# Optimization experiments

Hardware: AMD Instinct MI355X
Metric: run time of the kernel (lower is better)

The kernel has to match this reference:

```python
import jax, jax.numpy as jnp
from jax import lax
import numpy as np

C_IN = 64
C_OUT = 64
CQ = C_OUT // 8   # query/key channels
K = 5             # axial kernel length
RATIO = 0.7       # hybrid-norm mixing ratio
EPS = 1e-5
DN = ('NCHW', 'OIHW', 'NCHW')


def setup_inputs() -> dict:
    key = jax.random.key(0)
    ks = jax.random.split(key, 16)
    rn = lambda k, s, sc=0.05: jax.random.normal(k, s, dtype=jnp.float32) * sc
    return dict(
        x=jax.random.normal(ks[0], (4, C_IN, 256, 256), dtype=jnp.float32),
        hconv_w=rn(ks[1], (C_IN, 1, 1, K)), hconv_b=rn(ks[2], (C_IN,)),
        vconv_w=rn(ks[3], (C_IN, 1, K, 1)), vconv_b=rn(ks[4], (C_IN,)),
        pw_w=rn(ks[5], (C_OUT, C_IN)), pw_b=rn(ks[6], (C_OUT,)),
        bn_w=1.0 + rn(ks[7], (C_OUT,)), bn_b=rn(ks[8], (C_OUT,)),
        q_w=rn(ks[9], (CQ, C_OUT)), q_b=rn(ks[10], (CQ,)),
        k_w=rn(ks[11], (CQ, C_OUT)), k_b=rn(ks[12], (CQ,)),
        v_w=rn(ks[13], (C_OUT, C_OUT)), v_b=rn(ks[14], (C_OUT,)),
        gamma=rn(ks[15], (1,), 0.1),
    )


def reference(x, hconv_w, hconv_b, vconv_w, vconv_b, pw_w, pw_b,
              bn_w, bn_b, q_w, q_b, k_w, k_b, v_w, v_b, gamma):
    # ---- AxialDepthwiseConv: depthwise (1,K) + (K,1) + x, relu, pointwise ----
    h = lax.conv_general_dilated(x, hconv_w, (1, 1), [(0, 0), (K // 2, K // 2)],
                                 dimension_numbers=DN, feature_group_count=C_IN)
    h = h + hconv_b[:, None, None]
    v = lax.conv_general_dilated(x, vconv_w, (1, 1), [(K // 2, K // 2), (0, 0)],
                                 dimension_numbers=DN, feature_group_count=C_IN)
    v = v + vconv_b[:, None, None]
    a = jax.nn.relu(h + v + x)
    y = jnp.einsum('bchw,oc->bohw', a, pw_w) + pw_b[:, None, None]

    # ---- HybridNormalization: 0.7*InstanceNorm(no affine) + 0.3*BatchNorm(train) ----
    im = y.mean((2, 3), keepdims=True)
    iv = y.var((2, 3), keepdims=True)
    inn = (y - im) * lax.rsqrt(iv + EPS)
    bm = y.mean((0, 2, 3), keepdims=True)
    bv = y.var((0, 2, 3), keepdims=True)
    bnn = (y - bm) * lax.rsqrt(bv + EPS) * bn_w[:, None, None] + bn_b[:, None, None]
    y = RATIO * inn + (1.0 - RATIO) * bnn

    # ---- CrissCrossAttention ----
    q = jnp.einsum('bchw,oc->bohw', y, q_w) + q_b[:, None, None]   # (B,CQ,H,W)
    k = jnp.einsum('bchw,oc->bohw', y, k_w) + k_b[:, None, None]   # (B,CQ,H,W)
    val = jnp.einsum('bchw,oc->bohw', y, v_w) + v_b[:, None, None] # (B,C,H,W)

    # height (per column w): attn[b,w,j,i] = softmax_i( q[b,:,j,w] . k[b,:,i,w] )
    Ah = jax.nn.softmax(jnp.einsum('bcjw,bciw->bwji', q, k), axis=-1)
    # h_out[b,c,i,w] = sum_j val[b,c,j,w] * Ah[b,w,j,i]  (matches bmm(value, attn))
    h_out = jnp.einsum('bcjw,bwji->bciw', val, Ah)

    # width (per row h): attn[b,h,y,x] = softmax_x( q[b,:,h,y] . k[b,:,h,x] )
    Av = jax.nn.softmax(jnp.einsum('bchy,bchx->bhyx', q, k), axis=-1)
    v_out = jnp.einsum('bchy,bhyx->bchx', val, Av)

    out = gamma[0] * (h_out + v_out) + y

    # ---- MaxPool2d(2,2) ----
    down = lax.reduce_window(out, -jnp.inf, lax.max, (1, 1, 2, 2), (1, 1, 2, 2), 'VALID')
    return out, down
```

## Files before the change

kernel.cpp:

```cpp
#include <hip/hip_runtime.h>
#include <hip/hip_bf16.h>

#define Bn 4
#define Cc 64
#define CQn 8
#define Hh 256
#define Ww 256
#define PLANE 65536

typedef unsigned short ushortT;
typedef __attribute__((ext_vector_type(8))) unsigned short us8;
typedef __attribute__((ext_vector_type(4))) unsigned short us4;
typedef __attribute__((ext_vector_type(8))) __bf16 bf16x8;
typedef __attribute__((ext_vector_type(4))) float f32x4;

__device__ inline ushortT f2bf(float f) {
    __hip_bfloat16 h = __float2bfloat16(f);
    return *(ushortT*)&h;
}
__device__ inline float bf2f(ushortT u) {
    return __uint_as_float((unsigned)u << 16);
}
union BF8U { us8 u; bf16x8 b; uint4 w; };
__device__ inline us8 zero_us8() {
    BF8U z; z.w.x = 0; z.w.y = 0; z.w.z = 0; z.w.w = 0; return z.u;
}

__global__ __launch_bounds__(256) void dw_kernel(
    const float* __restrict__ x,
    const float* __restrict__ hw, const float* __restrict__ hb,
    const float* __restrict__ vw, const float* __restrict__ vb,
    ushortT* __restrict__ aout)
{
    int blk = blockIdx.x;
    int bc = blk >> 4;
    int ht = blk & 15;
    int h0 = ht * 16;
    int c = bc & 63;
    int tid = threadIdx.x;
    __shared__ float rows[20][260];
    const float* xp = x + (size_t)bc * PLANE;
    #pragma unroll
    for (int i = 0; i < 20; ++i) {
        int hr = h0 - 2 + i;
        rows[i][tid + 2] = (hr >= 0 && hr < Hh) ? xp[hr * Ww + tid] : 0.f;
    }
    if (tid < 20) {
        rows[tid][0] = 0.f; rows[tid][1] = 0.f;
        rows[tid][258] = 0.f; rows[tid][259] = 0.f;
    }
    __syncthreads();

    float hw0 = hw[c * 5 + 0], hw1 = hw[c * 5 + 1], hw2 = hw[c * 5 + 2],
          hw3 = hw[c * 5 + 3], hw4 = hw[c * 5 + 4];
    float vw0 = vw[c * 5 + 0], vw1 = vw[c * 5 + 1], vw2 = vw[c * 5 + 2],
          vw3 = vw[c * 5 + 3], vw4 = vw[c * 5 + 4];
    float bias = hb[c] + vb[c];

    ushortT* op = aout + (size_t)bc * PLANE + h0 * Ww + tid;
    #pragma unroll
    for (int r = 0; r < 16; ++r) {
        float hs = hw0 * rows[r + 2][tid]     + hw1 * rows[r + 2][tid + 1]
                 + hw2 * rows[r + 2][tid + 2] + hw3 * rows[r + 2][tid + 3]
                 + hw4 * rows[r + 2][tid + 4];
        float vs = vw0 * rows[r][tid + 2]     + vw1 * rows[r + 1][tid + 2]
                 + vw2 * rows[r + 2][tid + 2] + vw3 * rows[r + 3][tid + 2]
                 + vw4 * rows[r + 4][tid + 2];
        float res = hs + vs + bias + rows[r + 2][tid + 2];
        op[r * Ww] = f2bf(fmaxf(res, 0.f));
    }
}

__global__ __launch_bounds__(256) void pw_mfma_kernel(
    const ushortT* __restrict__ a_bf, const float* __restrict__ pwwf,
    const float* __restrict__ pwb,
    float* __restrict__ y_raw, float* __restrict__ sums, float* __restrict__ sumsq)
{
    int blk = blockIdx.x;
    int b = blk >> 8;
    int t0 = (blk & 255) << 8;
    int tid = threadIdx.x, lane = tid & 63, wv = tid >> 6;
    int half = lane >> 4;
    int col = lane & 15;

    __shared__ ushortT ytile[256 * 74];

    {
        size_t base = (size_t)b * Cc * PLANE + t0 + tid;
        uint* wrow = (uint*)&ytile[tid * 74];
        #pragma unroll
        for (int c = 0; c < Cc; c += 2) {
            ushortT v0 = a_bf[base + (size_t)c * PLANE];
            ushortT v1 = a_bf[base + (size_t)(c + 1) * PLANE];
            wrow[c >> 1] = (uint)v0 | ((uint)v1 << 16);
        }
    }
    __syncthreads();

    int m0 = wv * 16;
    BF8U a0, a1;
    {
        const float* wr = pwwf + (m0 + col) * 64 + half * 8;
        #pragma unroll
        for (int e = 0; e < 8; ++e) {
            a0.u[e] = f2bf(wr[e]);
            a1.u[e] = f2bf(wr[32 + e]);
        }
    }

    float bias[4], s[4], s2[4];
    #pragma unroll
    for (int r = 0; r < 4; ++r) {
        bias[r] = pwb[m0 + half * 4 + r];
        s[r] = 0.f; s2[r] = 0.f;
    }

    const uint* lw = (const uint*)ytile;
    #pragma unroll 4
    for (int t = 0; t < 16; ++t) {
        int rbase = (t * 16 + col) * 37 + half * 4;
        BF8U b0, b1;
        b0.w.x = lw[rbase];      b0.w.y = lw[rbase + 1];
        b0.w.z = lw[rbase + 2];  b0.w.w = lw[rbase + 3];
        b1.w.x = lw[rbase + 16]; b1.w.y = lw[rbase + 17];
        b1.w.z = lw[rbase + 18]; b1.w.w = lw[rbase + 19];
        f32x4 acc = (f32x4){0.f, 0.f, 0.f, 0.f};
        acc = __builtin_amdgcn_mfma_f32_16x16x32_bf16(a0.b, b0.b, acc, 0, 0, 0);
        acc = __builtin_amdgcn_mfma_f32_16x16x32_bf16(a1.b, b1.b, acc, 0, 0, 0);
        int pix = t * 16 + col;
        #pragma unroll
        for (int r = 0; r < 4; ++r) {
            int c = m0 + half * 4 + r;
            float v = acc[r] + bias[r];
            y_raw[(size_t)(b * Cc + c) * PLANE + t0 + pix] = v;
            s[r] += v; s2[r] += v * v;
        }
    }
    #pragma unroll
    for (int r = 0; r < 4; ++r) {
        #pragma unroll
        for (int d = 8; d > 0; d >>= 1) {
            s[r]  += __shfl_down(s[r], d, 16);
            s2[r] += __shfl_down(s2[r], d, 16);
        }
    }
    if (col == 0) {
        #pragma unroll
        for (int r = 0; r < 4; ++r) {
            int c = m0 + half * 4 + r;
            atomicAdd(&sums[b * Cc + c], s[r]);
            atomicAdd(&sumsq[b * Cc + c], s2[r]);
        }
    }
}

__global__ __launch_bounds__(256) void qkv_mfma_kernel(
    const float* __restrict__ y_raw,
    const float* __restrict__ sums, const float* __restrict__ sumsq,
    const float* __restrict__ bnw, const float* __restrict__ bnb,
    const float* __restrict__ qwf, const float* __restrict__ qbias,
    const float* __restrict__ kwf, const float* __restrict__ kbias,
    const float* __restrict__ vwf, const float* __restrict__ vbias,
    ushortT* __restrict__ q, ushortT* __restrict__ k,
    ushortT* __restrict__ val)
{
    int blk = blockIdx.x;
    int b = blk >> 8;
    int t0 = (blk & 255) << 8;
    int tid = threadIdx.x, lane = tid & 63, wv = tid >> 6;
    int half = lane >> 4;
    int col = lane & 15;

    __shared__ ushortT ytile[256 * 74];
    __shared__ float alpha_s[64], beta_s[64];

    if (tid < 64) {
        int c = tid;
        float im[4], e2[4];
        float bm = 0.f, be2 = 0.f;
        #pragma unroll
        for (int bb = 0; bb < 4; ++bb) {
            im[bb] = sums[bb * Cc + c] * (1.f / 65536.f);
            e2[bb] = sumsq[bb * Cc + c] * (1.f / 65536.f);
            bm += im[bb]; be2 += e2[bb];
        }
        bm *= 0.25f; be2 *= 0.25f;
        float rsb = rsqrtf(be2 - bm * bm + 1e-5f);
        float wgt = bnw[c];
        float rsi = rsqrtf(e2[b] - im[b] * im[b] + 1e-5f);
        alpha_s[c] = 0.7f * rsi + 0.3f * rsb * wgt;
        beta_s[c]  = -0.7f * im[b] * rsi - 0.3f * bm * rsb * wgt + 0.3f * bnb[c];
    }
    __syncthreads();

    {
        size_t base = (size_t)b * Cc * PLANE + t0 + tid;
        uint* wrow = (uint*)&ytile[tid * 74];
        #pragma unroll
        for (int c = 0; c < Cc; c += 2) {
            float v0 = y_raw[base + (size_t)c * PLANE];
            float v1 = y_raw[base + (size_t)(c + 1) * PLANE];
            float n0 = alpha_s[c] * v0 + beta_s[c];
            float n1 = alpha_s[c + 1] * v1 + beta_s[c + 1];
            wrow[c >> 1] = (uint)f2bf(n0) | ((uint)f2bf(n1) << 16);
        }
    }
    __syncthreads();

    const uint* lw = (const uint*)ytile;

    {
        const float* wr = (col < 8) ? (qwf + col * 64) : (kwf + (col - 8) * 64);
        BF8U a0, a1;
        #pragma unroll
        for (int e = 0; e < 8; ++e) {
            a0.u[e] = f2bf(wr[half * 8 + e]);
            a1.u[e] = f2bf(wr[32 + half * 8 + e]);
        }
        #pragma unroll
        for (int i = 0; i < 4; ++i) {
            int t = wv * 4 + i;
            int rbase = (t * 16 + col) * 37 + half * 4;
            BF8U b0, b1;
            b0.w.x = lw[rbase];      b0.w.y = lw[rbase + 1];
            b0.w.z = lw[rbase + 2];  b0.w.w = lw[rbase + 3];
            b1.w.x = lw[rbase + 16]; b1.w.y = lw[rbase + 17];
            b1.w.z = lw[rbase + 18]; b1.w.w = lw[rbase + 19];
            f32x4 acc = (f32x4){0.f, 0.f, 0.f, 0.f};
            acc = __builtin_amdgcn_mfma_f32_16x16x32_bf16(a0.b, b0.b, acc, 0, 0, 0);
            acc = __builtin_amdgcn_mfma_f32_16x16x32_bf16(a1.b, b1.b, acc, 0, 0, 0);
            int pix = t * 16 + col;
            #pragma unroll
            for (int r = 0; r < 4; ++r) {
                int row = half * 4 + r;
                if (row < 8)
                    q[(size_t)(b * CQn + row) * PLANE + t0 + pix] = f2bf(acc[r] + qbias[row]);
                else
                    k[(size_t)(b * CQn + row - 8) * PLANE + t0 + pix] = f2bf(acc[r] + kbias[row - 8]);
            }
        }
    }

    {
        int m0 = wv * 16;
        BF8U a0, a1;
        {
            const float* wr = vwf + (m0 + col) * 64 + half * 8;
            #pragma unroll
            for (int e = 0; e < 8; ++e) {
                a0.u[e] = f2bf(wr[e]);
                a1.u[e] = f2bf(wr[32 + e]);
            }
        }
        float bias[4];
        #pragma unroll
        for (int r = 0; r < 4; ++r) bias[r] = vbias[m0 + half * 4 + r];
        #pragma unroll 4
        for (int t = 0; t < 16; ++t) {
            int rbase = (t * 16 + col) * 37 + half * 4;
            BF8U b0, b1;
            b0.w.x = lw[rbase];      b0.w.y = lw[rbase + 1];
            b0.w.z = lw[rbase + 2];  b0.w.w = lw[rbase + 3];
            b1.w.x = lw[rbase + 16]; b1.w.y = lw[rbase + 17];
            b1.w.z = lw[rbase + 18]; b1.w.w = lw[rbase + 19];
            f32x4 acc = (f32x4){0.f, 0.f, 0.f, 0.f};
            acc = __builtin_amdgcn_mfma_f32_16x16x32_bf16(a0.b, b0.b, acc, 0, 0, 0);
            acc = __builtin_amdgcn_mfma_f32_16x16x32_bf16(a1.b, b1.b, acc, 0, 0, 0);
            int pix = t * 16 + col;
            #pragma unroll
            for (int r = 0; r < 4; ++r) {
                int c = m0 + half * 4 + r;
                val[(size_t)(b * Cc + c) * PLANE + t0 + pix] = f2bf(acc[r] + bias[r]);
            }
        }
    }
}

__global__ __launch_bounds__(256) void transpose_all_kernel(
    const ushortT* __restrict__ qb, ushortT* __restrict__ qT,
    const ushortT* __restrict__ kb, ushortT* __restrict__ kT,
    const ushortT* __restrict__ vb, ushortT* __restrict__ vT)
{
    int blk = blockIdx.x;
    int plane = blk >> 6;
    int tile = blk & 63;
    const ushortT* src; ushortT* dst;
    if (plane < 32)      { src = qb + (size_t)plane * PLANE;        dst = qT + (size_t)plane * PLANE; }
    else if (plane < 64) { src = kb + (size_t)(plane - 32) * PLANE; dst = kT + (size_t)(plane - 32) * PLANE; }
    else                 { src = vb + (size_t)(plane - 64) * PLANE; dst = vT + (size_t)(plane - 64) * PLANE; }
    int th = (tile >> 3) * 32;
    int tw = (tile & 7) * 32;
    __shared__ ushortT t[32][34];
    int lw = threadIdx.x & 31;
    int lh = threadIdx.x >> 5;
    #pragma unroll
    for (int i = 0; i < 4; ++i)
        t[lh + 8 * i][lw] = src[(th + lh + 8 * i) * Ww + tw + lw];
    __syncthreads();
    #pragma unroll
    for (int i = 0; i < 4; ++i)
        dst[(tw + lh + 8 * i) * Hh + th + lw] = t[lw][lh + 8 * i];
}

__global__ __launch_bounds__(256) void attn_kernel(
    const ushortT* __restrict__ q0, const ushortT* __restrict__ k0,
    const ushortT* __restrict__ v0, ushortT* __restrict__ o0,
    const ushortT* __restrict__ q1, const ushortT* __restrict__ k1,
    const ushortT* __restrict__ v1, ushortT* __restrict__ o1)
{
    int blk = blockIdx.x;
    int sel = blk >> 10;
    const ushortT* __restrict__ q   = sel ? q1 : q0;
    const ushortT* __restrict__ k   = sel ? k1 : k0;
    const ushortT* __restrict__ val = sel ? v1 : v0;
    ushortT* __restrict__ outp      = sel ? o1 : o0;
    int bblk = blk & 1023;
    int b = bblk >> 8;
    int r = bblk & 255;
    int tid = threadIdx.x;
    int lane = tid & 63;
    int wv = tid >> 6;
    int col = lane & 15;
    int quad = lane >> 4;

    __shared__ ushortT q_s[256 * 8];
    __shared__ ushortT k_s[256 * 8];
    __shared__ ushortT A_lds[4 * 256 * 8];
    __shared__ float mhat[256];
    __shared__ float shiftv[256];
    __shared__ float kred[32];

    size_t vbase = (size_t)b * Cc * PLANE + (size_t)r * Ww
                 + (size_t)(wv * 16 + col) * PLANE + quad * 8;
    BF8U afb[2];
    afb[0].u = *(const us8*)(val + vbase);

    size_t qkbase = (size_t)b * CQn * PLANE + (size_t)r * Ww + tid;
    float qf[8], ka[8];
    {
        BF8U qp, kp;
        #pragma unroll
        for (int c = 0; c < 8; ++c) {
            ushortT qv = q[qkbase + (size_t)c * PLANE];
            ushortT kv = k[qkbase + (size_t)c * PLANE];
            qp.u[c] = qv; kp.u[c] = kv;
            qf[c] = bf2f(qv);
            ka[c] = fabsf(bf2f(kv));
        }
        *(us8*)&q_s[tid * 8] = qp.u;
        *(us8*)&k_s[tid * 8] = kp.u;
    }
    #pragma unroll
    for (int d = 1; d < 64; d <<= 1)
        #pragma unroll
        for (int c = 0; c < 8; ++c)
            ka[c] = fmaxf(ka[c], __shfl_xor(ka[c], d));
    if (lane == 0)
        #pragma unroll
        for (int c = 0; c < 8; ++c) kred[wv * 8 + c] = ka[c];
    __syncthreads();

    {
        float mh = 0.f;
        #pragma unroll
        for (int c = 0; c < 8; ++c) {
            float km = fmaxf(fmaxf(kred[c], kred[8 + c]),
                             fmaxf(kred[16 + c], kred[24 + c]));
            mh += fabsf(qf[c]) * km;
        }
        mhat[tid] = mh;
    }
    __syncthreads();

    #pragma unroll
    for (int t = 0; t < 4; ++t) {
        int jt = wv * 4 + t;
        BF8U qa; qa.u = zero_us8();
        if (quad == 0) qa.u = *(const us8*)&q_s[(jt * 16 + col) * 8];
        float mh4[4];
        #pragma unroll
        for (int rr = 0; rr < 4; ++rr) mh4[rr] = mhat[jt * 16 + quad * 4 + rr];
        f32x4 ls = (f32x4){0.f, 0.f, 0.f, 0.f};
        for (int it = 0; it < 16; ++it) {
            BF8U kb;
            kb.u = *(const us8*)&k_s[(it * 16 + col) * 8];
            f32x4 sacc = (f32x4){0.f, 0.f, 0.f, 0.f};
            sacc = __builtin_amdgcn_mfma_f32_16x16x32_bf16(qa.b, kb.b, sacc, 0, 0, 0);
            #pragma unroll
            for (int rr = 0; rr < 4; ++rr)
                ls[rr] += __expf(sacc[rr] - mh4[rr]);
        }
        #pragma unroll
        for (int d = 1; d < 16; d <<= 1)
            #pragma unroll
            for (int rr = 0; rr < 4; ++rr)
                ls[rr] += __shfl_xor(ls[rr], d);
        if (col == 0)
            #pragma unroll
            for (int rr = 0; rr < 4; ++rr)
                shiftv[jt * 16 + quad * 4 + rr] = mh4[rr] + __logf(ls[rr]);
    }
    __syncthreads();

    BF8U kc[4];
    #pragma unroll
    for (int i = 0; i < 4; ++i)
        kc[i].u = *(const us8*)&k_s[((wv * 4 + i) * 16 + col) * 8];
    f32x4 acc[16];
    #pragma unroll
    for (int t = 0; t < 16; ++t) acc[t] = (f32x4){0.f, 0.f, 0.f, 0.f};

    #pragma unroll
    for (int ks = 0; ks < 8; ++ks) {
        if (ks < 7)
            afb[(ks + 1) & 1].u = *(const us8*)(val + vbase + (ks + 1) * 32);
        #pragma unroll
        for (int jj2 = 0; jj2 < 2; ++jj2) {
            int jt = ks * 2 + jj2;
            BF8U qa; qa.u = zero_us8();
            if (quad == 0) qa.u = *(const us8*)&q_s[(jt * 16 + col) * 8];
            float sh4[4];
            #pragma unroll
            for (int rr = 0; rr < 4; ++rr) sh4[rr] = shiftv[jt * 16 + quad * 4 + rr];
            #pragma unroll
            for (int i = 0; i < 4; ++i) {
                f32x4 sacc = (f32x4){0.f, 0.f, 0.f, 0.f};
                sacc = __builtin_amdgcn_mfma_f32_16x16x32_bf16(qa.b, kc[i].b, sacc, 0, 0, 0);
                us4 pk;
                #pragma unroll
                for (int rr = 0; rr < 4; ++rr)
                    pk[rr] = f2bf(__expf(sacc[rr] - sh4[rr]));
                int irow = (wv * 4 + i) * 16 + col;
                int jq = jj2 * 2 + (quad >> 1);
                *(us4*)&A_lds[(jq * 256 + irow) * 8 + (quad & 1) * 4] = pk;
            }
        }
        __syncthreads();
        #pragma unroll
        for (int t = 0; t < 16; ++t) {
            BF8U bfr;
            bfr.u = *(const us8*)&A_lds[(quad * 256 + t * 16 + col) * 8];
            acc[t] = __builtin_amdgcn_mfma_f32_16x16x32_bf16(afb[ks & 1].b, bfr.b, acc[t], 0, 0, 0);
        }
        __syncthreads();
    }

    size_t obase = (size_t)b * Cc * PLANE + (size_t)r * Ww;
    #pragma unroll
    for (int t = 0; t < 16; ++t) {
        int i = t * 16 + col;
        #pragma unroll
        for (int rr = 0; rr < 4; ++rr) {
            int c = wv * 16 + quad * 4 + rr;
            outp[obase + (size_t)c * PLANE + i] = f2bf(acc[t][rr]);
        }
    }
}

__global__ __launch_bounds__(256) void final_kernel(
    const ushortT* __restrict__ houtT, const ushortT* __restrict__ hout0,
    const float* __restrict__ y_raw,
    const float* __restrict__ sums, const float* __restrict__ sumsq,
    const float* __restrict__ bnw, const float* __restrict__ bnb,
    const float* __restrict__ gamma,
    float* __restrict__ out, float* __restrict__ down)
{
    int blk = blockIdx.x;
    int tile = blk & 63;
    int bc = blk >> 6;
    int b = bc >> 6;
    int c = bc & 63;
    int th = (tile >> 3) * 32;
    int tw = (tile & 7) * 32;

    float im[4], e2[4];
    float bm = 0.f, be2 = 0.f;
    #pragma unroll
    for (int bb = 0; bb < 4; ++bb) {
        im[bb] = sums[bb * Cc + c] * (1.f / 65536.f);
        e2[bb] = sumsq[bb * Cc + c] * (1.f / 65536.f);
        bm += im[bb]; be2 += e2[bb];
    }
    bm *= 0.25f; be2 *= 0.25f;
    float rsb = rsqrtf(be2 - bm * bm + 1e-5f);
    float wgt = bnw[c];
    float rsi = rsqrtf(e2[b] - im[b] * im[b] + 1e-5f);
    float al = 0.7f * rsi + 0.3f * rsb * wgt;
    float bt = -0.7f * im[b] * rsi - 0.3f * bm * rsb * wgt + 0.3f * bnb[c];

    __shared__ float t[32][33];
    const ushortT* hT = houtT + (size_t)bc * PLANE;
    {
        int ww = threadIdx.x >> 3;
        int hh = (threadIdx.x & 7) * 4;
        us4 v4 = *(const us4*)(hT + (size_t)(tw + ww) * Hh + th + hh);
        t[hh + 0][ww] = __uint_as_float((unsigned)v4[0] << 16);
        t[hh + 1][ww] = __uint_as_float((unsigned)v4[1] << 16);
        t[hh + 2][ww] = __uint_as_float((unsigned)v4[2] << 16);
        t[hh + 3][ww] = __uint_as_float((unsigned)v4[3] << 16);
    }
    __syncthreads();
    float g = gamma[0];
    int qw_ = threadIdx.x & 15;
    int qh_ = threadIdx.x >> 4;
    const float* yb = y_raw + (size_t)bc * PLANE;
    const ushortT* hb = hout0 + (size_t)bc * PLANE;
    float* ob = out + (size_t)bc * PLANE;
    float mx = -1e30f;
    float2 res[2];
    #pragma unroll
    for (int i = 0; i < 2; ++i) {
        int hh = 2 * qh_ + i;
        int off = (th + hh) * Ww + tw + 2 * qw_;
        uint hv = *(const uint*)(hb + off);
        float2 y = *(const float2*)(yb + off);
        float y0 = al * y.x + bt;
        float y1 = al * y.y + bt;
        float o0 = g * (t[hh][2 * qw_]     + bf2f((ushortT)(hv & 0xffff))) + y0;
        float o1 = g * (t[hh][2 * qw_ + 1] + bf2f((ushortT)(hv >> 16)))   + y1;
        res[i] = make_float2(o0, o1);
        mx = fmaxf(mx, fmaxf(o0, o1));
    }
    #pragma unroll
    for (int i = 0; i < 2; ++i) {
        int off = (th + 2 * qh_ + i) * Ww + tw + 2 * qw_;
        *(float2*)(ob + off) = res[i];
    }
    down[(size_t)bc * 16384 + (th / 2 + qh_) * 128 + tw / 2 + qw_] = mx;
}

extern "C" void kernel_launch(void* const* d_in, const int* in_sizes, int n_in,
                              void* d_out, int out_size, void* d_ws, size_t ws_size,
                              hipStream_t stream)
{
    const float* x     = (const float*)d_in[0];
    const float* hw    = (const float*)d_in[1];
    const float* hb    = (const float*)d_in[2];
    const float* vw    = (const float*)d_in[3];
    const float* vb    = (const float*)d_in[4];
    const float* pww   = (const float*)d_in[5];
    const float* pwb   = (const float*)d_in[6];
    const float* bnw   = (const float*)d_in[7];
    const float* bnb   = (const float*)d_in[8];
    const float* qw    = (const float*)d_in[9];
    const float* qb    = (const float*)d_in[10];
    const float* kw    = (const float*)d_in[11];
    const float* kb    = (const float*)d_in[12];
    const float* vw2   = (const float*)d_in[13];
    const float* vb2   = (const float*)d_in[14];
    const float* gamma = (const float*)d_in[15];

    float* ws = (float*)d_ws;
    const size_t NP = (size_t)Bn * Cc * PLANE;
    const size_t NQ = (size_t)Bn * CQn * PLANE;
    float* y_raw  = ws;
    float* slotB  = ws + NP;
    float* slotC  = ws + 2 * NP;
    float* slotD  = ws + 2 * NP + NP / 2;
    float* ptr    = ws + 3 * NP;
    ushortT* qbuf = (ushortT*)ptr;
    ushortT* kbuf = qbuf + NQ;
    ushortT* qT   = kbuf + NQ;
    ushortT* kT   = qT + NQ;
    float* sums   = (float*)(kT + NQ);
    float* sumsq  = sums + 256;

    ushortT* a_buf = (ushortT*)slotC;
    ushortT* valT  = (ushortT*)slotC;
    ushortT* valb  = (ushortT*)slotD;
    ushortT* hout0 = (ushortT*)slotB;
    ushortT* houtT = hout0 + NP;
    float* out  = (float*)d_out;
    float* down = out + NP;

    hipMemsetAsync(sums, 0, 512 * sizeof(float), stream);
    dw_kernel<<<dim3(Bn * Cc * 16), dim3(256), 0, stream>>>(
        x, hw, hb, vw, vb, a_buf);
    pw_mfma_kernel<<<dim3(Bn * 256), dim3(256), 0, stream>>>(
        a_buf, pww, pwb, y_raw, sums, sumsq);
    qkv_mfma_kernel<<<dim3(Bn * 256), dim3(256), 0, stream>>>(
        y_raw, sums, sumsq, bnw, bnb, qw, qb, kw, kb, vw2, vb2,
        qbuf, kbuf, valb);
    transpose_all_kernel<<<dim3(320 * 64), dim3(256), 0, stream>>>(
        qbuf, qT, kbuf, kT, valb, valT);
    attn_kernel<<<dim3(2 * Bn * Hh), dim3(256), 0, stream>>>(
        qbuf, kbuf, valb, hout0, qT, kT, valT, houtT);
    final_kernel<<<dim3(Bn * Cc * 64), dim3(256), 0, stream>>>(
        houtT, hout0, y_raw, sums, sumsq, bnw, bnb, gamma, out, down);
}
```

Before: 365.5 us.

## Store pointwise output in bf16, interleave q/k buffers, zero stats in-kernel

The pointwise conv output y is now stored as bf16 instead of fp32, which halves its write traffic and the reads of it in the qkv and final kernels. Query and key are written into one interleaved 16-channel buffer so attention reads them from one base pointer, and the transpose kernel handles a single q/k source. The memset of the statistics accumulators is replaced by block 0 of the depthwise kernel zeroing them. The final residual now adds a bf16-rounded y, which costs output precision, and relying on block 0 to finish zeroing before later kernels accumulate depends on kernel ordering in the stream.

```diff
diff --git a/kernel.cpp b/kernel.cpp
--- a/kernel.cpp
+++ b/kernel.cpp
@@ -30,14 +30,16 @@
     const float* __restrict__ x,
     const float* __restrict__ hw, const float* __restrict__ hb,
     const float* __restrict__ vw, const float* __restrict__ vb,
-    ushortT* __restrict__ aout)
+    ushortT* __restrict__ aout,
+    float* __restrict__ sums, float* __restrict__ sumsq)
 {
     int blk = blockIdx.x;
+    int tid = threadIdx.x;
+    if (blk == 0) { sums[tid] = 0.f; sumsq[tid] = 0.f; }
     int bc = blk >> 4;
     int ht = blk & 15;
     int h0 = ht * 16;
     int c = bc & 63;
-    int tid = threadIdx.x;
     __shared__ float rows[20][260];
     const float* xp = x + (size_t)bc * PLANE;
     #pragma unroll
@@ -74,7 +76,7 @@
 __global__ __launch_bounds__(256) void pw_mfma_kernel(
     const ushortT* __restrict__ a_bf, const float* __restrict__ pwwf,
     const float* __restrict__ pwb,
-    float* __restrict__ y_raw, float* __restrict__ sums, float* __restrict__ sumsq)
+    ushortT* __restrict__ y_bf, float* __restrict__ sums, float* __restrict__ sumsq)
 {
     int blk = blockIdx.x;
     int b = blk >> 8;
@@ -132,7 +134,7 @@
         for (int r = 0; r < 4; ++r) {
             int c = m0 + half * 4 + r;
             float v = acc[r] + bias[r];
-            y_raw[(size_t)(b * Cc + c) * PLANE + t0 + pix] = v;
+            y_bf[(size_t)(b * Cc + c) * PLANE + t0 + pix] = f2bf(v);
             s[r] += v; s2[r] += v * v;
         }
     }
@@ -155,14 +157,13 @@
 }
 
 __global__ __launch_bounds__(256) void qkv_mfma_kernel(
-    const float* __restrict__ y_raw,
+    const ushortT* __restrict__ y_bf,
     const float* __restrict__ sums, const float* __restrict__ sumsq,
     const float* __restrict__ bnw, const float* __restrict__ bnb,
     const float* __restrict__ qwf, const float* __restrict__ qbias,
     const float* __restrict__ kwf, const float* __restrict__ kbias,
     const float* __restrict__ vwf, const float* __restrict__ vbias,
-    ushortT* __restrict__ q, ushortT* __restrict__ k,
-    ushortT* __restrict__ val)
+    ushortT* __restrict__ qk, ushortT* __restrict__ val)
 {
     int blk = blockIdx.x;
     int b = blk >> 8;
@@ -198,8 +199,8 @@
         uint* wrow = (uint*)&ytile[tid * 74];
         #pragma unroll
         for (int c = 0; c < Cc; c += 2) {
-            float v0 = y_raw[base + (size_t)c * PLANE];
-            float v1 = y_raw[base + (size_t)(c + 1) * PLANE];
+            float v0 = bf2f(y_bf[base + (size_t)c * PLANE]);
+            float v1 = bf2f(y_bf[base + (size_t)(c + 1) * PLANE]);
             float n0 = alpha_s[c] * v0 + beta_s[c];
             float n1 = alpha_s[c + 1] * v1 + beta_s[c + 1];
             wrow[c >> 1] = (uint)f2bf(n0) | ((uint)f2bf(n1) << 16);
@@ -216,6 +217,12 @@
         for (int e = 0; e < 8; ++e) {
             a0.u[e] = f2bf(wr[half * 8 + e]);
             a1.u[e] = f2bf(wr[32 + half * 8 + e]);
+        }
+        float qkb4[4];
+        #pragma unroll
+        for (int r = 0; r < 4; ++r) {
+            int row = half * 4 + r;
+            qkb4[r] = (row < 8) ? qbias[row] : kbias[row - 8];
         }
         #pragma unroll
         for (int i = 0; i < 4; ++i) {
@@ -233,10 +240,7 @@
             #pragma unroll
             for (int r = 0; r < 4; ++r) {
                 int row = half * 4 + r;
-                if (row < 8)
-                    q[(size_t)(b * CQn + row) * PLANE + t0 + pix] = f2bf(acc[r] + qbias[row]);
-                else
-                    k[(size_t)(b * CQn + row - 8) * PLANE + t0 + pix] = f2bf(acc[r] + kbias[row - 8]);
+                qk[(size_t)(b * 16 + row) * PLANE + t0 + pix] = f2bf(acc[r] + qkb4[r]);
             }
         }
     }
@@ -277,17 +281,15 @@
 }
 
 __global__ __launch_bounds__(256) void transpose_all_kernel(
-    const ushortT* __restrict__ qb, ushortT* __restrict__ qT,
-    const ushortT* __restrict__ kb, ushortT* __restrict__ kT,
+    const ushortT* __restrict__ qkb, ushortT* __restrict__ qkT,
     const ushortT* __restrict__ vb, ushortT* __restrict__ vT)
 {
     int blk = blockIdx.x;
     int plane = blk >> 6;
     int tile = blk & 63;
     const ushortT* src; ushortT* dst;
-    if (plane < 32)      { src = qb + (size_t)plane * PLANE;        dst = qT + (size_t)plane * PLANE; }
-    else if (plane < 64) { src = kb + (size_t)(plane - 32) * PLANE; dst = kT + (size_t)(plane - 32) * PLANE; }
-    else                 { src = vb + (size_t)(plane - 64) * PLANE; dst = vT + (size_t)(plane - 64) * PLANE; }
+    if (plane < 64) { src = qkb + (size_t)plane * PLANE;        dst = qkT + (size_t)plane * PLANE; }
+    else            { src = vb + (size_t)(plane - 64) * PLANE;  dst = vT + (size_t)(plane - 64) * PLANE; }
     int th = (tile >> 3) * 32;
     int tw = (tile & 7) * 32;
     __shared__ ushortT t[32][34];
@@ -303,15 +305,14 @@
 }
 
 __global__ __launch_bounds__(256) void attn_kernel(
-    const ushortT* __restrict__ q0, const ushortT* __restrict__ k0,
-    const ushortT* __restrict__ v0, ushortT* __restrict__ o0,
-    const ushortT* __restrict__ q1, const ushortT* __restrict__ k1,
-    const ushortT* __restrict__ v1, ushortT* __restrict__ o1)
+    const ushortT* __restrict__ qk0, const ushortT* __restrict__ v0,
+    ushortT* __restrict__ o0,
+    const ushortT* __restrict__ qk1, const ushortT* __restrict__ v1,
+    ushortT* __restrict__ o1)
 {
     int blk = blockIdx.x;
     int sel = blk >> 10;
-    const ushortT* __restrict__ q   = sel ? q1 : q0;
-    const ushortT* __restrict__ k   = sel ? k1 : k0;
+    const ushortT* __restrict__ qk  = sel ? qk1 : qk0;
     const ushortT* __restrict__ val = sel ? v1 : v0;
     ushortT* __restrict__ outp      = sel ? o1 : o0;
     int bblk = blk & 1023;
@@ -335,14 +336,14 @@
     BF8U afb[2];
     afb[0].u = *(const us8*)(val + vbase);
 
-    size_t qkbase = (size_t)b * CQn * PLANE + (size_t)r * Ww + tid;
+    size_t qkbase = (size_t)b * 16 * PLANE + (size_t)r * Ww + tid;
     float qf[8], ka[8];
     {
         BF8U qp, kp;
         #pragma unroll
         for (int c = 0; c < 8; ++c) {
-            ushortT qv = q[qkbase + (size_t)c * PLANE];
-            ushortT kv = k[qkbase + (size_t)c * PLANE];
+            ushortT qv = qk[qkbase + (size_t)c * PLANE];
+            ushortT kv = qk[qkbase + (size_t)(8 + c) * PLANE];
             qp.u[c] = qv; kp.u[c] = kv;
             qf[c] = bf2f(qv);
             ka[c] = fabsf(bf2f(kv));
@@ -459,7 +460,7 @@
 
 __global__ __launch_bounds__(256) void final_kernel(
     const ushortT* __restrict__ houtT, const ushortT* __restrict__ hout0,
-    const float* __restrict__ y_raw,
+    const ushortT* __restrict__ y_bf,
     const float* __restrict__ sums, const float* __restrict__ sumsq,
     const float* __restrict__ bnw, const float* __restrict__ bnb,
     const float* __restrict__ gamma,
@@ -503,7 +504,7 @@
     float g = gamma[0];
     int qw_ = threadIdx.x & 15;
     int qh_ = threadIdx.x >> 4;
-    const float* yb = y_raw + (size_t)bc * PLANE;
+    const ushortT* yb = y_bf + (size_t)bc * PLANE;
     const ushortT* hb = hout0 + (size_t)bc * PLANE;
     float* ob = out + (size_t)bc * PLANE;
     float mx = -1e30f;
@@ -513,9 +514,9 @@
         int hh = 2 * qh_ + i;
         int off = (th + hh) * Ww + tw + 2 * qw_;
         uint hv = *(const uint*)(hb + off);
-        float2 y = *(const float2*)(yb + off);
-        float y0 = al * y.x + bt;
-        float y1 = al * y.y + bt;
+        uint yv = *(const uint*)(yb + off);
+        float y0 = al * bf2f((ushortT)(yv & 0xffff)) + bt;
+        float y1 = al * bf2f((ushortT)(yv >> 16))   + bt;
         float o0 = g * (t[hh][2 * qw_]     + bf2f((ushortT)(hv & 0xffff))) + y0;
         float o1 = g * (t[hh][2 * qw_ + 1] + bf2f((ushortT)(hv >> 16)))   + y1;
         res[i] = make_float2(o0, o1);
@@ -553,16 +554,14 @@
     float* ws = (float*)d_ws;
     const size_t NP = (size_t)Bn * Cc * PLANE;
     const size_t NQ = (size_t)Bn * CQn * PLANE;
-    float* y_raw  = ws;
+    ushortT* y_bf = (ushortT*)ws;
     float* slotB  = ws + NP;
     float* slotC  = ws + 2 * NP;
     float* slotD  = ws + 2 * NP + NP / 2;
     float* ptr    = ws + 3 * NP;
-    ushortT* qbuf = (ushortT*)ptr;
-    ushortT* kbuf = qbuf + NQ;
-    ushortT* qT   = kbuf + NQ;
-    ushortT* kT   = qT + NQ;
-    float* sums   = (float*)(kT + NQ);
+    ushortT* qkbuf = (ushortT*)ptr;
+    ushortT* qkT   = qkbuf + 2 * NQ;
+    float* sums   = (float*)(qkT + 2 * NQ);
     float* sumsq  = sums + 256;
 
     ushortT* a_buf = (ushortT*)slotC;
@@ -573,18 +572,17 @@
     float* out  = (float*)d_out;
     float* down = out + NP;
 
-    hipMemsetAsync(sums, 0, 512 * sizeof(float), stream);
     dw_kernel<<<dim3(Bn * Cc * 16), dim3(256), 0, stream>>>(
-        x, hw, hb, vw, vb, a_buf);
+        x, hw, hb, vw, vb, a_buf, sums, sumsq);
     pw_mfma_kernel<<<dim3(Bn * 256), dim3(256), 0, stream>>>(
-        a_buf, pww, pwb, y_raw, sums, sumsq);
+        a_buf, pww, pwb, y_bf, sums, sumsq);
     qkv_mfma_kernel<<<dim3(Bn * 256), dim3(256), 0, stream>>>(
-        y_raw, sums, sumsq, bnw, bnb, qw, qb, kw, kb, vw2, vb2,
-        qbuf, kbuf, valb);
+        y_bf, sums, sumsq, bnw, bnb, qw, qb, kw, kb, vw2, vb2,
+        qkbuf, valb);
     transpose_all_kernel<<<dim3(320 * 64), dim3(256), 0, stream>>>(
-        qbuf, qT, kbuf, kT, valb, valT);
+        qkbuf, qkT, valb, valT);
     attn_kernel<<<dim3(2 * Bn * Hh), dim3(256), 0, stream>>>(
-        qbuf, kbuf, valb, hout0, qT, kT, valT, houtT);
+        qkbuf, valb, hout0, qkT, valT, houtT);
     final_kernel<<<dim3(Bn * Cc * 64), dim3(256), 0, stream>>>(
-        houtT, hout0, y_raw, sums, sumsq, bnw, bnb, gamma, out, down);
-}
+        houtT, hout0, y_bf, sums, sumsq, bnw, bnb, gamma, out, down);
+}
```

Measured after the change: 354.4 us. 1.03x faster.
